# Kernel optimization log

Measured on AMD Instinct MI355X. Metric: run time of the kernel, lower is better.

The kernel has to match this reference:

```python
import jax, jax.numpy as jnp
import numpy as np
import math

B, T, D = 2, 1024, 256
N, H = 1024, 8
HD = N // H
K = 32
STEPS = 2
VOCAB = 32000
TWO_PI = 2.0 * math.pi


def _ln(x, g, b):
    mu = x.mean(-1, keepdims=True)
    var = ((x - mu) ** 2).mean(-1, keepdims=True)
    return (x - mu) / jnp.sqrt(var + 1e-5) * g + b


def _gelu(x):
    # torch nn.GELU default = exact erf form
    return jax.nn.gelu(x, approximate=False)


def _forward(tokens, emb, field_init, Wq, Wv, mW1, mb1, mW2, mb2, base_metric,
             decoder, hebbian, fW1, fb1, fW2, fb2, g1, b1, g2, b2, gf, bf, Wl, bl):
    x = emb[tokens] + field_init  # [B,T,D]
    # quantized RoPE (BDH): freqs quantized in pairs, phases mod 1
    freqs = 1.0 / (2.0 ** 16) ** (jnp.floor(jnp.arange(D) / 2) * 2.0 / D) / TWO_PI  # [D]
    phases = (jnp.arange(T, dtype=jnp.float32)[:, None] * freqs[None, :]) % 1.0 * TWO_PI  # [T,D]
    cos, sin = jnp.cos(phases)[None], jnp.sin(phases)[None]
    x_rot = jnp.stack([-x[..., 1::2], x[..., ::2]], axis=-1).reshape(x.shape)
    x = x * cos + x_rot * sin

    # window j of token t covers padded positions t..t+K-1 == original t-(K-1)..t (causal)
    win_idx = jnp.arange(T)[:, None] + jnp.arange(K)[None, :]  # [T,K]

    def interaction(y):
        qs = jax.nn.relu(jnp.einsum('btd,hde->bthe', y, Wq))  # [B,T,H,HD] sparse query
        vs = jax.nn.relu(jnp.einsum('btd,hde->bthe', y, Wv))  # [B,T,H,HD] sparse value
        # dynamic diagonal metric from field signature
        qf = qs.reshape(B, T, N)
        sig = qf.mean(1) + qf[:, ::8].mean(1) * 0.5  # T >= 8 branch
        mod = _gelu(sig @ mW1 + mb1) @ mW2 + mb2  # [B,H*HD]
        metric = jax.nn.softplus(base_metric[None] + 0.1 * mod.reshape(B, H, HD)) + 1e-6
        # causal k-window extraction (unfold equivalent)
        qp = jnp.pad(qs, ((0, 0), (K - 1, 0), (0, 0), (0, 0)))
        vp = jnp.pad(vs, ((0, 0), (K - 1, 0), (0, 0), (0, 0)))
        qw = qp[:, win_idx].transpose(0, 1, 3, 2, 4)  # [B,T,H,K,HD]
        vw = vp[:, win_idx].transpose(0, 1, 3, 2, 4)
        diff = qs[:, :, :, None, :] - qw
        dist = jnp.sqrt(jnp.sum(metric[:, None, :, None, :] * diff ** 2, -1) + 1e-8)  # [B,T,H,K]
        infl = jnp.exp(-dist)
        infl = infl / (infl.sum(-1, keepdims=True) + 1e-8)
        ctx = jnp.einsum('bthk,bthkd->bthd', infl, vw)
        # Hebbian memory contraction (eval mode: state is fixed buffer)
        qn = qs / jnp.maximum(jnp.linalg.norm(qs, axis=-1, keepdims=True), 1e-12)
        ctx = ctx + jnp.einsum('bthd,hde->bthe', qn, hebbian)
        # multiplicative gating + decode
        return (qs * ctx).reshape(B, T, N) @ decoder

    for _ in range(STEPS):  # fixed evolution steps (eval, dropout off)
        dx = interaction(_ln(x, g1, b1)) + (_gelu(_ln(x, g2, b2) @ fW1 + fb1) @ fW2 + fb2)
        x = x + dx
    return _ln(x, gf, bf) @ Wl + bl  # [B,T,VOCAB]


def setup_inputs() -> dict:
    key = jax.random.key(0)
    ks = jax.random.split(key, 12)
    s = 0.02
    return {
        'tokens': jax.random.randint(ks[0], (B, T), 0, VOCAB),
        'emb': jax.random.normal(ks[1], (VOCAB, D)) * s,
        'field_init': jax.random.normal(ks[2], (1, 1, D)) * s,
        'Wq': jax.random.normal(ks[3], (H, D, HD)) * s,
        'Wv': jax.random.normal(ks[4], (H, D, HD)) * s,
        'mW1': jax.random.normal(ks[5], (N, N // 2)) * s,
        'mb1': jnp.zeros((N // 2,)),
        'mW2': jax.random.normal(ks[6], (N // 2, H * HD)) * s,
        'mb2': jnp.zeros((H * HD,)),
        'base_metric': jnp.ones((H, HD)) * 0.1,
        'decoder': jax.random.normal(ks[7], (N, D)) * s,
        'hebbian': jax.random.normal(ks[8], (H, HD, HD)) * 0.01,
        'fW1': jax.random.normal(ks[9], (D, 4 * D)) * s,
        'fb1': jnp.zeros((4 * D,)),
        'fW2': jax.random.normal(ks[10], (4 * D, D)) * s,
        'fb2': jnp.zeros((D,)),
        'g1': jnp.ones((D,)), 'b1': jnp.zeros((D,)),
        'g2': jnp.ones((D,)), 'b2': jnp.zeros((D,)),
        'gf': jnp.ones((D,)), 'bf': jnp.zeros((D,)),
        'Wl': jax.random.normal(ks[11], (D, VOCAB)) * s,
        'bl': jnp.zeros((VOCAB,)),
    }


def reference(tokens, emb, field_init, Wq, Wv, mW1, mb1, mW2, mb2, base_metric,
              decoder, hebbian, fW1, fb1, fW2, fb2, g1, b1, g2, b2, gf, bf, Wl, bl):
    return _forward(tokens, emb, field_init, Wq, Wv, mW1, mb1, mW2, mb2, base_metric,
                    decoder, hebbian, fW1, fb1, fW2, fb2, g1, b1, g2, b2, gf, bf, Wl, bl)
```

## Files before the change

kernel.cpp:

```cpp
#include <hip/hip_runtime.h>
#include <hip/hip_bf16.h>
#include <math.h>

#define B_ 2
#define T_ 1024
#define D_ 256
#define N_ 1024
#define H_ 8
#define HD_ 128
#define K_ 32
#define VOCAB_ 32000

typedef __attribute__((ext_vector_type(8))) short short8v;
typedef __attribute__((ext_vector_type(4))) float f32x4;

static __device__ __forceinline__ float geluf(float x) {
    return 0.5f * x * (1.0f + erff(x * 0.70710678118654752f));
}

static __device__ __forceinline__ ushort f2bf(float f) {
    unsigned u = __builtin_bit_cast(unsigned, f);
    u += 0x7fff + ((u >> 16) & 1);
    return (ushort)(u >> 16);
}

static __device__ __forceinline__ float bf2f(ushort u) {
    unsigned v = ((unsigned)u) << 16;
    return __builtin_bit_cast(float, v);
}

__global__ void embed_rope_ln_kernel(const int* __restrict__ tokens,
                                     const float* __restrict__ emb,
                                     const float* __restrict__ field_init,
                                     const float* __restrict__ g1, const float* __restrict__ b1,
                                     const float* __restrict__ g2, const float* __restrict__ b2,
                                     float* __restrict__ x,
                                     ushort* __restrict__ y1, ushort* __restrict__ y2) {
    int bt = blockIdx.x;
    int d = threadIdx.x;
    int t = bt & (T_ - 1);
    int tok = tokens[bt];
    float v = emb[(long)tok * D_ + d] + field_init[d];
    float partner = __shfl_xor(v, 1);
    float rot = (d & 1) ? partner : -partner;
    float freq = exp2f(-0.0625f * (float)(d & ~1)) * (1.0f / 6.283185307179586f);
    float ph = fmodf((float)t * freq, 1.0f) * 6.283185307179586f;
    v = v * cosf(ph) + rot * sinf(ph);
    long i = (long)bt * D_ + d;
    x[i] = v;
    __shared__ float red[4];
    int lane = d & 63, wid = d >> 6;
    float s = v;
    #pragma unroll
    for (int off = 32; off; off >>= 1) s += __shfl_xor(s, off);
    if (lane == 0) red[wid] = s;
    __syncthreads();
    float mu = (red[0] + red[1] + red[2] + red[3]) * (1.0f / D_);
    float dv = v - mu;
    float s2 = dv * dv;
    #pragma unroll
    for (int off = 32; off; off >>= 1) s2 += __shfl_xor(s2, off);
    __syncthreads();
    if (lane == 0) red[wid] = s2;
    __syncthreads();
    float var = (red[0] + red[1] + red[2] + red[3]) * (1.0f / D_);
    float rstd = rsqrtf(var + 1e-5f);
    float nv = dv * rstd;
    y1[i] = f2bf(nv * g1[d] + b1[d]);
    y2[i] = f2bf(nv * g2[d] + b2[d]);
}

__global__ void ln_kernel(float* __restrict__ x,
                          const float* __restrict__ addA, const float* __restrict__ addB,
                          const float* __restrict__ g1, const float* __restrict__ b1,
                          const float* __restrict__ g2, const float* __restrict__ b2,
                          ushort* __restrict__ y1, ushort* __restrict__ y2) {
    int row = blockIdx.x;
    int d = threadIdx.x;
    long i = (long)row * D_ + d;
    float v = x[i] + addA[i] + addB[i];
    x[i] = v;
    __shared__ float red[4];
    int lane = d & 63, wid = d >> 6;
    float s = v;
    #pragma unroll
    for (int off = 32; off; off >>= 1) s += __shfl_xor(s, off);
    if (lane == 0) red[wid] = s;
    __syncthreads();
    float mu = (red[0] + red[1] + red[2] + red[3]) * (1.0f / D_);
    float dv = v - mu;
    float s2 = dv * dv;
    #pragma unroll
    for (int off = 32; off; off >>= 1) s2 += __shfl_xor(s2, off);
    __syncthreads();
    if (lane == 0) red[wid] = s2;
    __syncthreads();
    float var = (red[0] + red[1] + red[2] + red[3]) * (1.0f / D_);
    float rstd = rsqrtf(var + 1e-5f);
    float nv = dv * rstd;
    y1[i] = f2bf(nv * g1[d] + b1[d]);
    if (y2) y2[i] = f2bf(nv * g2[d] + b2[d]);
}

static __device__ __forceinline__ void tcast_tile(
    const float* __restrict__ in, ushort* __restrict__ out,
    int R, int C, int ry, int cx) {
    __shared__ float sm[64][65];
    int r0 = ry * 64, c0 = cx * 64;
    int tx = threadIdx.x & 63, ty = threadIdx.x >> 6;
    #pragma unroll
    for (int i = 0; i < 16; ++i) {
        int r = i * 4 + ty;
        sm[r][tx] = in[(long)(r0 + r) * C + c0 + tx];
    }
    __syncthreads();
    #pragma unroll
    for (int i = 0; i < 16; ++i) {
        int c = i * 4 + ty;
        out[(long)(c0 + c) * R + r0 + tx] = f2bf(sm[tx][c]);
    }
}

__global__ __launch_bounds__(256) void tcast_kernel(
    const float* __restrict__ in, ushort* __restrict__ out, int R, int C) {
    tcast_tile(in, out, R, C, blockIdx.y, blockIdx.x);
}

struct TcastBatch {
    const float* in[8];
    ushort* out[8];
    long inS[8], outS[8];
    int cb[8], rb[8], R[8], C[8];
    int cum[9];
};

__global__ __launch_bounds__(256) void tcast_all_kernel(TcastBatch tb) {
    int bid = blockIdx.x;
    int d = 0;
    #pragma unroll
    for (int i = 0; i < 8; ++i) if (bid >= tb.cum[i + 1]) d = i + 1;
    int local = bid - tb.cum[d];
    int bpz = tb.cb[d] * tb.rb[d];
    int z = local / bpz;
    int rem = local - z * bpz;
    int cx = rem % tb.cb[d], ry = rem / tb.cb[d];
    tcast_tile(tb.in[d] + z * tb.inS[d], tb.out[d] + z * tb.outS[d],
               tb.R[d], tb.C[d], ry, cx);
}

#define LDK 72
#define CSTR 132

template<int ACT, int OUTBF, int SIG>
__device__ __forceinline__ void gemm128_core(
    const ushort* __restrict__ A, int lda,
    const ushort* __restrict__ Bt, int ldb,
    const float* __restrict__ bias, void* __restrict__ Cout, int ldc,
    int Kd, int bx, int by,
    float* __restrict__ psOut, float* __restrict__ ps8Out) {
    __shared__ __align__(16) ushort As[128 * LDK];
    __shared__ __align__(16) ushort Bs[128 * LDK];
    int tid = threadIdx.x;
    int wid = tid >> 6, lane = tid & 63;
    int brow = by * 128, bcol = bx * 128;
    int wr = wid >> 1, wc = wid & 1;
    f32x4 acc[4][4] = {};
    for (int k0 = 0; k0 < Kd; k0 += 64) {
        __syncthreads();
        #pragma unroll
        for (int j = 0; j < 4; ++j) {
            int idx = tid + j * 256;
            int r = idx >> 3, sgm = idx & 7;
            *(short8v*)&As[r * LDK + sgm * 8] =
                *(const short8v*)&A[(long)(brow + r) * lda + k0 + sgm * 8];
            *(short8v*)&Bs[r * LDK + sgm * 8] =
                *(const short8v*)&Bt[(long)(bcol + r) * ldb + k0 + sgm * 8];
        }
        __syncthreads();
        #pragma unroll
        for (int kk = 0; kk < 2; ++kk) {
            short8v af[4], bfv[4];
            #pragma unroll
            for (int m = 0; m < 4; ++m)
                af[m] = *(const short8v*)&As[(wr * 64 + m * 16 + (lane & 15)) * LDK + kk * 32 + (lane >> 4) * 8];
            #pragma unroll
            for (int n = 0; n < 4; ++n)
                bfv[n] = *(const short8v*)&Bs[(wc * 64 + n * 16 + (lane & 15)) * LDK + kk * 32 + (lane >> 4) * 8];
            #pragma unroll
            for (int m = 0; m < 4; ++m)
                #pragma unroll
                for (int n = 0; n < 4; ++n)
                    acc[m][n] = __builtin_amdgcn_mfma_f32_16x16x32_bf16(af[m], bfv[n], acc[m][n], 0, 0, 0);
        }
    }
    float* Cs = (float*)As;
    float cs = 0.f, cs8 = 0.f;
    #pragma unroll
    for (int chunk = 0; chunk < 4; ++chunk) {
        __syncthreads();
        if (wr == (chunk >> 1)) {
            #pragma unroll
            for (int mm = 0; mm < 2; ++mm) {
                int m = (chunk & 1) * 2 + mm;
                int lr0 = mm * 16 + ((lane >> 4) << 2);
                #pragma unroll
                for (int n = 0; n < 4; ++n) {
                    int lcol = wc * 64 + n * 16 + (lane & 15);
                    #pragma unroll
                    for (int j = 0; j < 4; ++j)
                        Cs[(lr0 + j) * CSTR + lcol] = acc[m][n][j];
                }
            }
        }
        __syncthreads();
        int lrow = tid >> 3, f4 = tid & 7;
        long grow = brow + chunk * 32 + lrow;
        if (OUTBF) {
            #pragma unroll
            for (int u = 0; u < 2; ++u) {
                int c0i = (f4 + u * 8) * 8;
                uint pk[4];
                #pragma unroll
                for (int q = 0; q < 4; ++q) {
                    int cc = c0i + 2 * q;
                    float v0 = Cs[lrow * CSTR + cc]     + (bias ? bias[bcol + cc] : 0.0f);
                    float v1 = Cs[lrow * CSTR + cc + 1] + (bias ? bias[bcol + cc + 1] : 0.0f);
                    if (ACT == 1) { v0 = fmaxf(v0, 0.0f); v1 = fmaxf(v1, 0.0f); }
                    else if (ACT == 2) { v0 = geluf(v0); v1 = geluf(v1); }
                    pk[q] = (uint)f2bf(v0) | ((uint)f2bf(v1) << 16);
                }
                *(uint4*)&((ushort*)Cout)[grow * ldc + bcol + c0i] = *(uint4*)pk;
            }
        } else {
            #pragma unroll
            for (int u = 0; u < 4; ++u) {
                int c0i = (f4 + u * 8) * 4;
                float vv[4];
                #pragma unroll
                for (int q = 0; q < 4; ++q) {
                    float v = Cs[lrow * CSTR + c0i + q] + (bias ? bias[bcol + c0i + q] : 0.0f);
                    if (ACT == 1) v = fmaxf(v, 0.0f);
                    else if (ACT == 2) v = geluf(v);
                    vv[q] = v;
                }
                *(float4*)&((float*)Cout)[grow * ldc + bcol + c0i] = *(float4*)vv;
            }
        }
        if (SIG && tid < 128) {
            #pragma unroll
            for (int r = 0; r < 32; ++r) {
                float vr = fmaxf(Cs[r * CSTR + tid], 0.0f);
                cs += vr;
                if ((r & 7) == 0) cs8 += vr;
            }
        }
    }
    if (SIG && tid < 128) {
        psOut[by * 1024 + bcol + tid] = cs;
        ps8Out[by * 1024 + bcol + tid] = cs8;
    }
}

__global__ __launch_bounds__(256) void gemm3_kernel(
    const ushort* __restrict__ y1, const ushort* __restrict__ y2,
    const ushort* __restrict__ WqT, const ushort* __restrict__ WvT, const ushort* __restrict__ fW1T,
    const float* __restrict__ fb1,
    ushort* __restrict__ qs, ushort* __restrict__ vs, ushort* __restrict__ ffnh,
    float* __restrict__ ps, float* __restrict__ ps8) {
    int z = blockIdx.z;
    if (z == 0)
        gemm128_core<1, 1, 1>(y1, 256, WqT, 256, nullptr, qs, 1024, 256,
                              blockIdx.x, blockIdx.y, ps, ps8);
    else if (z == 1)
        gemm128_core<1, 1, 0>(y1, 256, WvT, 256, nullptr, vs, 1024, 256,
                              blockIdx.x, blockIdx.y, nullptr, nullptr);
    else
        gemm128_core<2, 1, 0>(y2, 256, fW1T, 256, fb1, ffnh, 1024, 256,
                              blockIdx.x, blockIdx.y, nullptr, nullptr);
}

__global__ __launch_bounds__(256) void vocab_kernel(
    const ushort* __restrict__ yf, const ushort* __restrict__ WlT,
    const float* __restrict__ bl, float* __restrict__ out) {
    int g = blockIdx.x;
    int nid = (g & 7) * 500 + (g >> 3);
    gemm128_core<0, 0, 0>(yf, 256, WlT, 256, bl, out, VOCAB_, 256,
                          nid >> 4, nid & 15, nullptr, nullptr);
}

__global__ __launch_bounds__(256) void gemm2_kernel(
    const ushort* __restrict__ gated, const ushort* __restrict__ ffnh,
    const ushort* __restrict__ decT, const ushort* __restrict__ fW2T,
    const float* __restrict__ fb2,
    float* __restrict__ dec_out, float* __restrict__ ffn_out) {
    int z = blockIdx.z;
    const ushort* A = z ? ffnh : gated;
    const ushort* Bt = z ? fW2T : decT;
    const float* bias = z ? fb2 : nullptr;
    float* C = z ? ffn_out : dec_out;
    const int Kd = 1024, N = 256;
    __shared__ __align__(16) ushort As[64 * LDK];
    __shared__ __align__(16) ushort Bs[64 * LDK];
    int tid = threadIdx.x;
    int wid = tid >> 6, lane = tid & 63;
    int brow = blockIdx.y * 64, bcol = blockIdx.x * 64;
    int wr = wid >> 1, wc = wid & 1;
    f32x4 acc[2][2] = {};
    for (int k0 = 0; k0 < Kd; k0 += 64) {
        __syncthreads();
        #pragma unroll
        for (int j = 0; j < 2; ++j) {
            int idx = tid + j * 256;
            int r = idx >> 3, sgm = idx & 7;
            *(short8v*)&As[r * LDK + sgm * 8] =
                *(const short8v*)&A[(long)(brow + r) * Kd + k0 + sgm * 8];
            *(short8v*)&Bs[r * LDK + sgm * 8] =
                *(const short8v*)&Bt[(long)(bcol + r) * Kd + k0 + sgm * 8];
        }
        __syncthreads();
        #pragma unroll
        for (int kk = 0; kk < 2; ++kk) {
            short8v af[2], bfv[2];
            #pragma unroll
            for (int m = 0; m < 2; ++m)
                af[m] = *(const short8v*)&As[(wr * 32 + m * 16 + (lane & 15)) * LDK + kk * 32 + (lane >> 4) * 8];
            #pragma unroll
            for (int n = 0; n < 2; ++n)
                bfv[n] = *(const short8v*)&Bs[(wc * 32 + n * 16 + (lane & 15)) * LDK + kk * 32 + (lane >> 4) * 8];
            #pragma unroll
            for (int m = 0; m < 2; ++m)
                #pragma unroll
                for (int n = 0; n < 2; ++n)
                    acc[m][n] = __builtin_amdgcn_mfma_f32_16x16x32_bf16(af[m], bfv[n], acc[m][n], 0, 0, 0);
        }
    }
    int r0 = brow + wr * 32 + ((lane >> 4) << 2);
    int c0 = bcol + wc * 32 + (lane & 15);
    #pragma unroll
    for (int n = 0; n < 2; ++n) {
        int col = c0 + n * 16;
        float bv = bias ? bias[col] : 0.0f;
        #pragma unroll
        for (int m = 0; m < 2; ++m)
            #pragma unroll
            for (int j = 0; j < 4; ++j)
                C[(long)(r0 + m * 16 + j) * N + col] = acc[m][n][j] + bv;
    }
}

__global__ __launch_bounds__(256) void mlp1_kernel(
    const float* __restrict__ ps, const float* __restrict__ ps8,
    const ushort* __restrict__ mW1T, const float* __restrict__ mb1,
    float* __restrict__ hid) {
    int blk = blockIdx.x;
    int b = blk >> 7;
    __shared__ float sig_l[1024];
    int tid = threadIdx.x;
    for (int c = tid; c < 1024; c += 256) {
        float s = 0.f, s8 = 0.f;
        #pragma unroll
        for (int by8 = 0; by8 < 8; ++by8) {
            s += ps[(b * 8 + by8) * 1024 + c];
            s8 += ps8[(b * 8 + by8) * 1024 + c];
        }
        sig_l[c] = s * (1.0f / 1024.0f) + 0.5f * s8 * (1.0f / 128.0f);
    }
    __syncthreads();
    int wv = tid >> 6, lane = tid & 63;
    int j = (blk & 127) * 4 + wv;
    const ushort* wrow = mW1T + (long)j * 1024;
    float acc = 0.f;
    #pragma unroll
    for (int c2 = 0; c2 < 4; ++c2) {
        int n0 = c2 * 256 + lane * 4;
        float4 sv = *(const float4*)&sig_l[n0];
        ushort4 w4 = *(const ushort4*)&wrow[n0];
        acc += bf2f(w4.x) * sv.x + bf2f(w4.y) * sv.y
             + bf2f(w4.z) * sv.z + bf2f(w4.w) * sv.w;
    }
    #pragma unroll
    for (int off = 32; off; off >>= 1) acc += __shfl_xor(acc, off);
    if (lane == 0) hid[b * 512 + j] = geluf(acc + mb1[j]);
}

__global__ __launch_bounds__(256) void mlp2_kernel(
    const float* __restrict__ hid, const ushort* __restrict__ mW2T,
    const float* __restrict__ mb2, const float* __restrict__ base_metric,
    float* __restrict__ metric) {
    int widx = blockIdx.x * 4 + (threadIdx.x >> 6);
    int b = widx >> 10, i = widx & 1023;
    int lane = threadIdx.x & 63;
    const float* hd = hid + b * 512;
    const ushort* w = mW2T + (long)i * 512;
    int j0 = lane * 8;
    short8v wv = *(const short8v*)&w[j0];
    float4 h0 = *(const float4*)&hd[j0];
    float4 h1 = *(const float4*)&hd[j0 + 4];
    float acc = bf2f((ushort)wv[0]) * h0.x + bf2f((ushort)wv[1]) * h0.y
              + bf2f((ushort)wv[2]) * h0.z + bf2f((ushort)wv[3]) * h0.w
              + bf2f((ushort)wv[4]) * h1.x + bf2f((ushort)wv[5]) * h1.y
              + bf2f((ushort)wv[6]) * h1.z + bf2f((ushort)wv[7]) * h1.w;
    #pragma unroll
    for (int off = 32; off; off >>= 1) acc += __shfl_xor(acc, off);
    if (lane == 0) {
        float v = base_metric[i] + 0.1f * (acc + mb2[i]);
        float sp = fmaxf(v, 0.f) + log1pf(expf(-fabsf(v)));
        metric[b * 1024 + i] = sp + 1e-6f;
    }
}

#define WLDR 67

__global__ __launch_bounds__(256) void window_kernel(
    const ushort* __restrict__ qs, const ushort* __restrict__ vs,
    const float* __restrict__ metric, const ushort* __restrict__ hebT,
    ushort* __restrict__ gated) {
    int tile = blockIdx.x, h = blockIdx.y, b = blockIdx.z;
    int t0 = tile * 32;
    int tid = threadIdx.x;
    __shared__ uint Qw[63 * WLDR];
    __shared__ uint Vw[63 * WLDR];
    __shared__ uint Qr[32 * 64];
    __shared__ float smf[HD_];
    if (tid < HD_) smf[tid] = sqrtf(metric[(b * H_ + h) * HD_ + tid]);
    __syncthreads();
    for (int i = tid; i < 63 * 64; i += 256) {
        int r = i >> 6, c = i & 63;
        int grow = t0 - 31 + r;
        uint qv = 0, vv = 0;
        if (grow >= 0) {
            long base = ((long)(b * T_ + grow) * N_ + h * HD_) >> 1;
            qv = ((const uint*)qs)[base + c];
            vv = ((const uint*)vs)[base + c];
        }
        float q0 = bf2f((ushort)(qv & 0xffff)) * smf[2 * c];
        float q1 = bf2f((ushort)(qv >> 16)) * smf[2 * c + 1];
        Qw[r * WLDR + c] = (uint)f2bf(q0) | ((uint)f2bf(q1) << 16);
        Vw[r * WLDR + c] = vv;
        if (r >= 31) Qr[(r - 31) * 64 + c] = qv;
    }
    __syncthreads();
    int w = tid >> 6, lane = tid & 63;
    int k = lane & 31, half = lane >> 5;
    float invn[8];
    #pragma unroll
    for (int ri = 0; ri < 8; ++ri) {
        uint u = Qr[(w * 8 + ri) * 64 + lane];
        float a0 = bf2f((ushort)(u & 0xffff)), a1 = bf2f((ushort)(u >> 16));
        float nv = a0 * a0 + a1 * a1;
        #pragma unroll
        for (int off = 32; off; off >>= 1) nv += __shfl_xor(nv, off);
        invn[ri] = 1.0f / fmaxf(sqrtf(nv), 1e-12f);
    }
    const ushort* hb = hebT + (long)h * HD_ * HD_;
    float hacc0[8] = {}, hacc1[8] = {};
    for (int dv = 0; dv < 16; ++dv) {
        short8v h0 = *(const short8v*)&hb[(2 * lane) * HD_ + dv * 8];
        short8v h1 = *(const short8v*)&hb[(2 * lane + 1) * HD_ + dv * 8];
        #pragma unroll
        for (int ri = 0; ri < 8; ++ri) {
            uint4 qu = *(const uint4*)&Qr[(w * 8 + ri) * 64 + dv * 4];
            float qd[8] = {bf2f((ushort)(qu.x & 0xffff)), bf2f((ushort)(qu.x >> 16)),
                           bf2f((ushort)(qu.y & 0xffff)), bf2f((ushort)(qu.y >> 16)),
                           bf2f((ushort)(qu.z & 0xffff)), bf2f((ushort)(qu.z >> 16)),
                           bf2f((ushort)(qu.w & 0xffff)), bf2f((ushort)(qu.w >> 16))};
            #pragma unroll
            for (int j = 0; j < 8; ++j) {
                hacc0[ri] = fmaf(qd[j], bf2f((ushort)h0[j]), hacc0[ri]);
                hacc1[ri] = fmaf(qd[j], bf2f((ushort)h1[j]), hacc1[ri]);
            }
        }
    }
    #pragma unroll 2
    for (int i = 0; i < 8; ++i) {
        int lt = w * 8 + i;
        int t = t0 + lt;
        const uint* qtrow = &Qw[(lt + 31) * WLDR + half * 32];
        const uint* qsrow = &Qw[(lt + k) * WLDR + half * 32];
        float val = 0.f;
        #pragma unroll
        for (int j = 0; j < 32; ++j) {
            uint a = qtrow[j], s = qsrow[j];
            float d0 = bf2f((ushort)(a & 0xffff)) - bf2f((ushort)(s & 0xffff));
            float d1 = bf2f((ushort)(a >> 16)) - bf2f((ushort)(s >> 16));
            val = fmaf(d0, d0, val);
            val = fmaf(d1, d1, val);
        }
        val += __shfl_xor(val, 32);
        float infl = __expf(-sqrtf(val + 1e-8f));
        float ws = infl;
        #pragma unroll
        for (int off = 16; off; off >>= 1) ws += __shfl_xor(ws, off);
        float wk = infl / (ws + 1e-8f);
        float c0 = hacc0[i] * invn[i], c1 = hacc1[i] * invn[i];
        #pragma unroll
        for (int kk = 0; kk < 32; ++kk) {
            float wkk = __shfl(wk, kk);
            uint vu = Vw[(lt + kk) * WLDR + lane];
            c0 = fmaf(wkk, bf2f((ushort)(vu & 0xffff)), c0);
            c1 = fmaf(wkk, bf2f((ushort)(vu >> 16)), c1);
        }
        uint qo = Qr[lt * 64 + lane];
        float g0 = bf2f((ushort)(qo & 0xffff)) * c0;
        float g1 = bf2f((ushort)(qo >> 16)) * c1;
        long rowb = (long)(b * T_ + t) * N_ + h * HD_;
        *(uint*)&gated[rowb + 2 * lane] = (uint)f2bf(g0) | ((uint)f2bf(g1) << 16);
    }
}

extern "C" void kernel_launch(void* const* d_in, const int* in_sizes, int n_in,
                              void* d_out, int out_size, void* d_ws, size_t ws_size,
                              hipStream_t stream) {
    const int*   tokens      = (const int*)  d_in[0];
    const float* emb         = (const float*)d_in[1];
    const float* field_init  = (const float*)d_in[2];
    const float* Wq          = (const float*)d_in[3];
    const float* Wv          = (const float*)d_in[4];
    const float* mW1         = (const float*)d_in[5];
    const float* mb1         = (const float*)d_in[6];
    const float* mW2         = (const float*)d_in[7];
    const float* mb2         = (const float*)d_in[8];
    const float* base_metric = (const float*)d_in[9];
    const float* decoder     = (const float*)d_in[10];
    const float* hebbian     = (const float*)d_in[11];
    const float* fW1         = (const float*)d_in[12];
    const float* fb1         = (const float*)d_in[13];
    const float* fW2         = (const float*)d_in[14];
    const float* fb2         = (const float*)d_in[15];
    const float* g1          = (const float*)d_in[16];
    const float* b1          = (const float*)d_in[17];
    const float* g2          = (const float*)d_in[18];
    const float* b2          = (const float*)d_in[19];
    const float* gf          = (const float*)d_in[20];
    const float* bf          = (const float*)d_in[21];
    const float* Wl          = (const float*)d_in[22];
    const float* bl          = (const float*)d_in[23];
    float* out = (float*)d_out;

    char* wp = (char*)d_ws;
    auto alloc = [&](size_t bytes) { char* p = wp; wp += (bytes + 255) & ~255UL; return p; };
    float*  x        = (float*) alloc(524288 * 4);
    ushort* y1_bf    = (ushort*)alloc(524288 * 2);
    ushort* y2_bf    = (ushort*)alloc(524288 * 2);
    ushort* yf_bf    = (ushort*)alloc(524288 * 2);
    ushort* qs_bf    = (ushort*)alloc(2097152 * 2);
    ushort* vs_bf    = (ushort*)alloc(2097152 * 2);
    ushort* gated_bf = (ushort*)alloc(2097152 * 2);
    ushort* ffnh_bf  = (ushort*)alloc(2097152 * 2);
    float*  dec_out  = (float*) alloc(524288 * 4);
    float*  ffn_out  = (float*) alloc(524288 * 4);
    ushort* WqT      = (ushort*)alloc(262144 * 2);
    ushort* WvT      = (ushort*)alloc(262144 * 2);
    ushort* decT     = (ushort*)alloc(262144 * 2);
    ushort* fW1T     = (ushort*)alloc(262144 * 2);
    ushort* fW2T     = (ushort*)alloc(262144 * 2);
    ushort* mW1T     = (ushort*)alloc(524288 * 2);
    ushort* mW2T     = (ushort*)alloc(524288 * 2);
    ushort* hebT     = (ushort*)alloc(131072 * 2);
    float*  ps       = (float*) alloc(16 * 1024 * 4);
    float*  ps8      = (float*) alloc(16 * 1024 * 4);
    float*  hid      = (float*) alloc(1024 * 4);
    float*  metricb  = (float*) alloc(2048 * 4);
    ushort* WlT      = (ushort*)qs_bf;

    TcastBatch tb;
    const float* tin[8]  = {Wq, Wv, decoder, fW1, fW2, mW1, mW2, hebbian};
    ushort*      tout[8] = {WqT, WvT, decT, fW1T, fW2T, mW1T, mW2T, hebT};
    long tinS[8]  = {256 * 128, 256 * 128, 0, 0, 0, 0, 0, 128 * 128};
    long toutS[8] = {128 * 256, 128 * 256, 0, 0, 0, 0, 0, 128 * 128};
    int tR[8] = {256, 256, 1024, 256, 1024, 1024, 512, 128};
    int tC[8] = {128, 128, 256, 1024, 256, 512, 1024, 128};
    int cum = 0;
    tb.cum[0] = 0;
    for (int i = 0; i < 8; ++i) {
        tb.in[i] = tin[i]; tb.out[i] = tout[i];
        tb.inS[i] = tinS[i]; tb.outS[i] = toutS[i];
        tb.R[i] = tR[i]; tb.C[i] = tC[i];
        tb.cb[i] = tC[i] / 64; tb.rb[i] = tR[i] / 64;
        int zc = (i == 0 || i == 1 || i == 7) ? 8 : 1;
        cum += tb.cb[i] * tb.rb[i] * zc;
        tb.cum[i + 1] = cum;
    }
    tcast_all_kernel<<<cum, 256, 0, stream>>>(tb);

    embed_rope_ln_kernel<<<B_ * T_, 256, 0, stream>>>(
        tokens, emb, field_init, g1, b1, g2, b2, x, y1_bf, y2_bf);

    for (int step = 0; step < 2; ++step) {
        if (step == 1)
            ln_kernel<<<B_ * T_, 256, 0, stream>>>(
                x, dec_out, ffn_out, g1, b1, g2, b2, y1_bf, y2_bf);
        gemm3_kernel<<<dim3(8, 16, 3), 256, 0, stream>>>(
            y1_bf, y2_bf, WqT, WvT, fW1T, fb1, qs_bf, vs_bf, ffnh_bf, ps, ps8);
        mlp1_kernel<<<256, 256, 0, stream>>>(ps, ps8, mW1T, mb1, hid);
        mlp2_kernel<<<512, 256, 0, stream>>>(hid, mW2T, mb2, base_metric, metricb);
        window_kernel<<<dim3(T_ / 32, H_, B_), 256, 0, stream>>>(
            qs_bf, vs_bf, metricb, hebT, gated_bf);
        gemm2_kernel<<<dim3(4, 32, 2), 256, 0, stream>>>(
            gated_bf, ffnh_bf, decT, fW2T, fb2, dec_out, ffn_out);
    }
    ln_kernel<<<B_ * T_, 256, 0, stream>>>(
        x, dec_out, ffn_out, gf, bf, nullptr, nullptr, yf_bf, nullptr);
    tcast_kernel<<<dim3(500, 4), 256, 0, stream>>>(Wl, WlT, 256, VOCAB_);
    vocab_kernel<<<4000, 256, 0, stream>>>(yf_bf, WlT, bl, out);
}
```

Measured before the change: 312.9 us.

## Rewrite window kernel with MFMA for distances, Hebbian product and weighted V sum

Restructures the causal-window attention kernel to use bf16 MFMA instructions. Metric-scaled distances are computed as norms minus twice a Gram matrix, and the Hebbian projection and the influence-weighted value sum are also done as matrix multiplies. The tile size drops from 32 to 16 tokens, which doubles the grid, and V is stored transposed in LDS. The intent is to replace scalar FMA loops with matrix-core work. In exchange, the Gram-form distance can lose precision, normalized weights are rounded to bf16, and the smaller tiles reload more overlapping window rows per output.

```diff
diff --git a/kernel.cpp b/kernel.cpp
--- a/kernel.cpp
+++ b/kernel.cpp
@@ -409,102 +409,154 @@
     }
 }
 
-#define WLDR 67
+#define QLD 136
+#define QLDU 68
+#define VLD 72
+#define PLD 72
+#define CLD 132
 
 __global__ __launch_bounds__(256) void window_kernel(
     const ushort* __restrict__ qs, const ushort* __restrict__ vs,
     const float* __restrict__ metric, const ushort* __restrict__ hebT,
     ushort* __restrict__ gated) {
     int tile = blockIdx.x, h = blockIdx.y, b = blockIdx.z;
-    int t0 = tile * 32;
+    int t0 = tile * 16;
     int tid = threadIdx.x;
-    __shared__ uint Qw[63 * WLDR];
-    __shared__ uint Vw[63 * WLDR];
-    __shared__ uint Qr[32 * 64];
-    __shared__ float smf[HD_];
-    if (tid < HD_) smf[tid] = sqrtf(metric[(b * H_ + h) * HD_ + tid]);
-    __syncthreads();
-    for (int i = tid; i < 63 * 64; i += 256) {
+    __shared__ __align__(16) ushort Qt[48 * QLD];
+    __shared__ __align__(16) ushort Qr[16 * QLD];
+    __shared__ __align__(16) ushort Vt[128 * VLD];
+    __shared__ __align__(16) ushort P[16 * PLD];
+    __shared__ float ctx[16 * CLD];
+    __shared__ float ns[48], invn_l[16], part[3][16], smf[128];
+
+    if (tid < 128) smf[tid] = sqrtf(metric[(b * H_ + h) * HD_ + tid]);
+    if (tid < 128) { int t = tid >> 3, c = tid & 7; ((uint*)P)[t * 36 + 24 + c] = 0; }
+    __syncthreads();
+
+    for (int i = tid; i < 48 * 64; i += 256) {
         int r = i >> 6, c = i & 63;
         int grow = t0 - 31 + r;
-        uint qv = 0, vv = 0;
-        if (grow >= 0) {
-            long base = ((long)(b * T_ + grow) * N_ + h * HD_) >> 1;
-            qv = ((const uint*)qs)[base + c];
-            vv = ((const uint*)vs)[base + c];
-        }
+        uint qv = 0;
+        if (r < 47 && grow >= 0)
+            qv = ((const uint*)qs)[(((long)(b * T_ + grow) * N_ + h * HD_) >> 1) + c];
         float q0 = bf2f((ushort)(qv & 0xffff)) * smf[2 * c];
         float q1 = bf2f((ushort)(qv >> 16)) * smf[2 * c + 1];
-        Qw[r * WLDR + c] = (uint)f2bf(q0) | ((uint)f2bf(q1) << 16);
-        Vw[r * WLDR + c] = vv;
-        if (r >= 31) Qr[(r - 31) * 64 + c] = qv;
-    }
-    __syncthreads();
+        ((uint*)Qt)[r * QLDU + c] = (uint)f2bf(q0) | ((uint)f2bf(q1) << 16);
+        if (r >= 31 && r < 47) ((uint*)Qr)[(r - 31) * QLDU + c] = qv;
+    }
+    for (int i = tid; i < 32 * 64; i += 256) {
+        int r2 = i >> 6, c = i & 63;
+        int ra = 2 * r2, rb_ = 2 * r2 + 1;
+        int ga = t0 - 31 + ra, gb = t0 - 31 + rb_;
+        uint v0 = 0, v1 = 0;
+        if (ra < 47 && ga >= 0)
+            v0 = ((const uint*)vs)[(((long)(b * T_ + ga) * N_ + h * HD_) >> 1) + c];
+        if (rb_ < 47 && gb >= 0)
+            v1 = ((const uint*)vs)[(((long)(b * T_ + gb) * N_ + h * HD_) >> 1) + c];
+        ((uint*)Vt)[(2 * c) * 36 + r2]     = (v0 & 0xffff) | ((v1 & 0xffff) << 16);
+        ((uint*)Vt)[(2 * c + 1) * 36 + r2] = (v0 >> 16) | (v1 & 0xffff0000u);
+    }
+    __syncthreads();
+
     int w = tid >> 6, lane = tid & 63;
-    int k = lane & 31, half = lane >> 5;
-    float invn[8];
-    #pragma unroll
-    for (int ri = 0; ri < 8; ++ri) {
-        uint u = Qr[(w * 8 + ri) * 64 + lane];
+    int lc = lane & 15, lr = lane >> 4;
+
+    for (int rr = 0; rr < 16; ++rr) {
+        int row = w * 16 + rr;
+        uint u = (row < 48) ? ((uint*)Qt)[row * QLDU + lane]
+                            : ((uint*)Qr)[(row - 48) * QLDU + lane];
         float a0 = bf2f((ushort)(u & 0xffff)), a1 = bf2f((ushort)(u >> 16));
         float nv = a0 * a0 + a1 * a1;
         #pragma unroll
         for (int off = 32; off; off >>= 1) nv += __shfl_xor(nv, off);
-        invn[ri] = 1.0f / fmaxf(sqrtf(nv), 1e-12f);
-    }
+        if (lane == 0) {
+            if (row < 48) ns[row] = nv;
+            else invn_l[row - 48] = 1.0f / fmaxf(sqrtf(nv), 1e-12f);
+        }
+    }
+    __syncthreads();
+
+    f32x4 accS = {};
+    if (w < 3) {
+        #pragma unroll
+        for (int k = 0; k < 4; ++k) {
+            short8v a = *(const short8v*)&Qt[(w * 16 + lc) * QLD + k * 32 + lr * 8];
+            short8v bf_ = *(const short8v*)&Qt[(31 + lc) * QLD + k * 32 + lr * 8];
+            accS = __builtin_amdgcn_mfma_f32_16x16x32_bf16(a, bf_, accS, 0, 0, 0);
+        }
+    }
+    f32x4 accH[2] = {};
     const ushort* hb = hebT + (long)h * HD_ * HD_;
-    float hacc0[8] = {}, hacc1[8] = {};
-    for (int dv = 0; dv < 16; ++dv) {
-        short8v h0 = *(const short8v*)&hb[(2 * lane) * HD_ + dv * 8];
-        short8v h1 = *(const short8v*)&hb[(2 * lane + 1) * HD_ + dv * 8];
-        #pragma unroll
-        for (int ri = 0; ri < 8; ++ri) {
-            uint4 qu = *(const uint4*)&Qr[(w * 8 + ri) * 64 + dv * 4];
-            float qd[8] = {bf2f((ushort)(qu.x & 0xffff)), bf2f((ushort)(qu.x >> 16)),
-                           bf2f((ushort)(qu.y & 0xffff)), bf2f((ushort)(qu.y >> 16)),
-                           bf2f((ushort)(qu.z & 0xffff)), bf2f((ushort)(qu.z >> 16)),
-                           bf2f((ushort)(qu.w & 0xffff)), bf2f((ushort)(qu.w >> 16))};
-            #pragma unroll
-            for (int j = 0; j < 8; ++j) {
-                hacc0[ri] = fmaf(qd[j], bf2f((ushort)h0[j]), hacc0[ri]);
-                hacc1[ri] = fmaf(qd[j], bf2f((ushort)h1[j]), hacc1[ri]);
-            }
-        }
-    }
-    #pragma unroll 2
-    for (int i = 0; i < 8; ++i) {
-        int lt = w * 8 + i;
-        int t = t0 + lt;
-        const uint* qtrow = &Qw[(lt + 31) * WLDR + half * 32];
-        const uint* qsrow = &Qw[(lt + k) * WLDR + half * 32];
-        float val = 0.f;
-        #pragma unroll
-        for (int j = 0; j < 32; ++j) {
-            uint a = qtrow[j], s = qsrow[j];
-            float d0 = bf2f((ushort)(a & 0xffff)) - bf2f((ushort)(s & 0xffff));
-            float d1 = bf2f((ushort)(a >> 16)) - bf2f((ushort)(s >> 16));
-            val = fmaf(d0, d0, val);
-            val = fmaf(d1, d1, val);
-        }
-        val += __shfl_xor(val, 32);
-        float infl = __expf(-sqrtf(val + 1e-8f));
-        float ws = infl;
-        #pragma unroll
-        for (int off = 16; off; off >>= 1) ws += __shfl_xor(ws, off);
-        float wk = infl / (ws + 1e-8f);
-        float c0 = hacc0[i] * invn[i], c1 = hacc1[i] * invn[i];
-        #pragma unroll
-        for (int kk = 0; kk < 32; ++kk) {
-            float wkk = __shfl(wk, kk);
-            uint vu = Vw[(lt + kk) * WLDR + lane];
-            c0 = fmaf(wkk, bf2f((ushort)(vu & 0xffff)), c0);
-            c1 = fmaf(wkk, bf2f((ushort)(vu >> 16)), c1);
-        }
-        uint qo = Qr[lt * 64 + lane];
-        float g0 = bf2f((ushort)(qo & 0xffff)) * c0;
-        float g1 = bf2f((ushort)(qo >> 16)) * c1;
-        long rowb = (long)(b * T_ + t) * N_ + h * HD_;
-        *(uint*)&gated[rowb + 2 * lane] = (uint)f2bf(g0) | ((uint)f2bf(g1) << 16);
+    #pragma unroll
+    for (int nt = 0; nt < 2; ++nt)
+        #pragma unroll
+        for (int k = 0; k < 4; ++k) {
+            short8v a = *(const short8v*)&Qr[lc * QLD + k * 32 + lr * 8];
+            short8v bf_ = *(const short8v*)&hb[(long)((w * 2 + nt) * 16 + lc) * HD_ + k * 32 + lr * 8];
+            accH[nt] = __builtin_amdgcn_mfma_f32_16x16x32_bf16(a, bf_, accH[nt], 0, 0, 0);
+        }
+    #pragma unroll
+    for (int nt = 0; nt < 2; ++nt)
+        #pragma unroll
+        for (int j = 0; j < 4; ++j) {
+            int t = lr * 4 + j;
+            ctx[t * CLD + (w * 2 + nt) * 16 + lc] = accH[nt][j] * invn_l[t];
+        }
+    float wgt[4];
+    if (w < 3) {
+        float nt_ = ns[31 + lc];
+        float psum = 0.f;
+        #pragma unroll
+        for (int j = 0; j < 4; ++j) {
+            int s = w * 16 + lr * 4 + j;
+            float val = fmaxf(nt_ + ns[s] - 2.0f * accS[j], 0.0f) + 1e-8f;
+            bool band = (s >= lc) && (s <= lc + 31);
+            wgt[j] = band ? __expf(-sqrtf(val)) : 0.0f;
+            psum += wgt[j];
+        }
+        psum += __shfl_xor(psum, 16);
+        psum += __shfl_xor(psum, 32);
+        if (lane < 16) part[w][lane] = psum;
+    }
+    __syncthreads();
+    if (w < 3) {
+        float inv = 1.0f / (part[0][lc] + part[1][lc] + part[2][lc] + 1e-8f);
+        uint lo = (uint)f2bf(wgt[0] * inv) | ((uint)f2bf(wgt[1] * inv) << 16);
+        uint hi = (uint)f2bf(wgt[2] * inv) | ((uint)f2bf(wgt[3] * inv) << 16);
+        uint2 pk = {lo, hi};
+        *(uint2*)&P[lc * PLD + w * 16 + lr * 4] = pk;
+    }
+    __syncthreads();
+    f32x4 accP[2] = {};
+    #pragma unroll
+    for (int mt = 0; mt < 2; ++mt)
+        #pragma unroll
+        for (int k = 0; k < 2; ++k) {
+            short8v a = *(const short8v*)&Vt[((w * 2 + mt) * 16 + lc) * VLD + k * 32 + lr * 8];
+            short8v bf_ = *(const short8v*)&P[lc * PLD + k * 32 + lr * 8];
+            accP[mt] = __builtin_amdgcn_mfma_f32_16x16x32_bf16(a, bf_, accP[mt], 0, 0, 0);
+        }
+    #pragma unroll
+    for (int mt = 0; mt < 2; ++mt)
+        #pragma unroll
+        for (int j = 0; j < 4; ++j) {
+            int e = (w * 2 + mt) * 16 + lr * 4 + j;
+            ctx[lc * CLD + e] += accP[mt][j];
+        }
+    __syncthreads();
+    {
+        int t = tid >> 4, g = tid & 15;
+        uint4 qu = *(const uint4*)&((const uint*)Qr)[t * QLDU + g * 4];
+        const float* crow = &ctx[t * CLD + g * 8];
+        uint qa[4] = {qu.x, qu.y, qu.z, qu.w};
+        uint outp[4];
+        #pragma unroll
+        for (int q4 = 0; q4 < 4; ++q4) {
+            float e0 = bf2f((ushort)(qa[q4] & 0xffff)) * crow[2 * q4];
+            float e1 = bf2f((ushort)(qa[q4] >> 16))   * crow[2 * q4 + 1];
+            outp[q4] = (uint)f2bf(e0) | ((uint)f2bf(e1) << 16);
+        }
+        *(uint4*)&gated[(long)(b * T_ + t0 + t) * N_ + h * HD_ + g * 8] = *(uint4*)outp;
     }
 }
 
@@ -594,7 +646,7 @@
             y1_bf, y2_bf, WqT, WvT, fW1T, fb1, qs_bf, vs_bf, ffnh_bf, ps, ps8);
         mlp1_kernel<<<256, 256, 0, stream>>>(ps, ps8, mW1T, mb1, hid);
         mlp2_kernel<<<512, 256, 0, stream>>>(hid, mW2T, mb2, base_metric, metricb);
-        window_kernel<<<dim3(T_ / 32, H_, B_), 256, 0, stream>>>(
+        window_kernel<<<dim3(T_ / 16, H_, B_), 256, 0, stream>>>(
             qs_bf, vs_bf, metricb, hebT, gated_bf);
         gemm2_kernel<<<dim3(4, 32, 2), 256, 0, stream>>>(
             gated_bf, ffnh_bf, decT, fW2T, fb2, dec_out, ffn_out);
```

After: 307.6 us. Within noise of the previous version (-1.7%).
